# Optimization experiments

Hardware: AMD Instinct MI355X
Metric: run time of the kernel (lower is better)

## Reference

```python
import jax, jax.numpy as jnp
import numpy as np

B, S, D, H, DFF = 4, 1024, 1024, 16, 4096
MAX_LEN = 1024
DK = D // H
EPS = 1e-5


def _ln(x, g, b):
    m = jnp.mean(x, axis=-1, keepdims=True)
    v = jnp.mean(jnp.square(x - m), axis=-1, keepdims=True)
    return (x - m) / jnp.sqrt(v + EPS) * g + b


def setup_inputs() -> dict:
    key = jax.random.key(0)
    ks = jax.random.split(key, 16)
    s = 0.02
    inp = {
        "x": jax.random.normal(ks[0], (B, S, D), jnp.float32),
        "wq": jax.random.normal(ks[1], (D, D), jnp.float32) * s,
        "bq": jnp.zeros((D,), jnp.float32),
        "wk": jax.random.normal(ks[2], (D, D), jnp.float32) * s,
        "bk": jnp.zeros((D,), jnp.float32),
        "wv": jax.random.normal(ks[3], (D, D), jnp.float32) * s,
        "bv": jnp.zeros((D,), jnp.float32),
        "wo": jax.random.normal(ks[4], (D, D), jnp.float32) * s,
        "bo": jnp.zeros((D,), jnp.float32),
        "rel_table": jax.random.normal(ks[5], (2 * MAX_LEN - 1, H), jnp.float32) * s,
        "ln1_g": jnp.ones((D,), jnp.float32),
        "ln1_b": jnp.zeros((D,), jnp.float32),
        "w1": jax.random.normal(ks[6], (D, DFF), jnp.float32) * s,
        "b1": jnp.zeros((DFF,), jnp.float32),
        "w2": jax.random.normal(ks[7], (DFF, D), jnp.float32) * s,
        "b2": jnp.zeros((D,), jnp.float32),
        "ln2_g": jnp.ones((D,), jnp.float32),
        "ln2_b": jnp.zeros((D,), jnp.float32),
        "mask": jnp.ones((B, 1, 1, S), jnp.int32),
    }
    return inp


def reference(x, wq, bq, wk, bk, wv, bv, wo, bo, rel_table,
              ln1_g, ln1_b, w1, b1, w2, b2, ln2_g, ln2_b, mask):
    # --- multi-head attention with relative position bias (post-LN encoder layer, eval mode) ---
    q = (x @ wq + bq).reshape(B, S, H, DK).transpose(0, 2, 1, 3)  # [B,H,S,dk]
    k = (x @ wk + bk).reshape(B, S, H, DK).transpose(0, 2, 1, 3)
    v = (x @ wv + bv).reshape(B, S, H, DK).transpose(0, 2, 1, 3)

    scores = jnp.einsum('bhqd,bhkd->bhqk', q, k) / jnp.sqrt(jnp.float32(DK))

    # relative position bias: table[(q - k + max_len - 1).clip] -> [1,H,S,S]
    coords = jnp.arange(S)[:, None] - jnp.arange(S)[None, :] + (MAX_LEN - 1)
    coords = jnp.clip(coords, 0, 2 * MAX_LEN - 2)
    bias = rel_table[coords]              # [S,S,H]
    scores = scores + bias.transpose(2, 0, 1)[None]

    scores = jnp.where(mask == 0, jnp.float32(-1e9), scores)
    attn = jax.nn.softmax(scores, axis=-1)
    ctx = jnp.einsum('bhqk,bhkd->bhqd', attn, v)
    ctx = ctx.transpose(0, 2, 1, 3).reshape(B, S, D)
    attn_out = ctx @ wo + bo

    x1 = _ln(x + attn_out, ln1_g, ln1_b)

    ff = jax.nn.relu(x1 @ w1 + b1) @ w2 + b2
    return _ln(x1 + ff, ln2_g, ln2_b)
```

## Files before the change

kernel.cpp:

```cpp
#include <hip/hip_runtime.h>
#include <hip/hip_bf16.h>

typedef __hip_bfloat16 bf16;
typedef __attribute__((ext_vector_type(8))) short short8;
typedef __attribute__((ext_vector_type(4))) float f32x4;

#define LOG2E 1.4426950408889634f

typedef const __attribute__((address_space(1))) void* gptr_t;
typedef __attribute__((address_space(3))) void* sptr_t;

__device__ __forceinline__ void async16(void* lds, const void* g) {
  __builtin_amdgcn_global_load_lds((gptr_t)g, (sptr_t)lds, 16, 0, 0);
}

__device__ __forceinline__ float bf2f(unsigned short u) {
  union { unsigned int i; float f; } c; c.i = ((unsigned int)u) << 16; return c.f;
}


__global__ __launch_bounds__(256) void cast_f2b_kernel(
    const float* __restrict__ src, bf16* __restrict__ dst, int n) {
  int i = (blockIdx.x * 256 + threadIdx.x) * 4;
  if (i >= n) return;
  float4 v = *(const float4*)(src + i);
  bf16 h4[4] = {__float2bfloat16(v.x), __float2bfloat16(v.y),
                __float2bfloat16(v.z), __float2bfloat16(v.w)};
  *(uint2*)((unsigned short*)dst + i) = *(uint2*)h4;
}

__global__ __launch_bounds__(256) void concat_bias(
    const float* __restrict__ bq, const float* __restrict__ bk,
    const float* __restrict__ bv, float* __restrict__ o) {
  int i = blockIdx.x * 256 + threadIdx.x;
  if (i >= 3072) return;
  o[i] = (i < 1024) ? bq[i] : (i < 2048 ? bk[i - 1024] : bv[i - 2048]);
}

__global__ __launch_bounds__(256) void transpose_f2b(
    const float* __restrict__ src, bf16* __restrict__ dst, int K, int N) {
  __shared__ float tl[32][33];
  int n0 = blockIdx.x * 32, k0 = blockIdx.y * 32;
  int tx = threadIdx.x, ty = threadIdx.y;
#pragma unroll
  for (int j = 0; j < 4; ++j)
    tl[ty + j * 8][tx] = src[(size_t)(k0 + ty + j * 8) * N + n0 + tx];
  __syncthreads();
#pragma unroll
  for (int j = 0; j < 4; ++j)
    dst[(size_t)(n0 + ty + j * 8) * K + k0 + tx] =
        __float2bfloat16(tl[tx][ty + j * 8]);
}

__global__ __launch_bounds__(256) void transpose4_f2b(
    const float* __restrict__ s0, const float* __restrict__ s1,
    const float* __restrict__ s2, const float* __restrict__ s3,
    bf16* __restrict__ d0, bf16* __restrict__ d1,
    bf16* __restrict__ d2, bf16* __restrict__ d3) {
  __shared__ float tl[32][33];
  const int z = blockIdx.z;
  const float* src = z == 0 ? s0 : z == 1 ? s1 : z == 2 ? s2 : s3;
  bf16* dst = z == 0 ? d0 : z == 1 ? d1 : z == 2 ? d2 : d3;
  int n0 = blockIdx.x * 32, k0 = blockIdx.y * 32;
  int tx = threadIdx.x, ty = threadIdx.y;
#pragma unroll
  for (int j = 0; j < 4; ++j)
    tl[ty + j * 8][tx] = src[(size_t)(k0 + ty + j * 8) * 1024 + n0 + tx];
  __syncthreads();
#pragma unroll
  for (int j = 0; j < 4; ++j)
    dst[(size_t)(n0 + ty + j * 8) * 1024 + k0 + tx] =
        __float2bfloat16(tl[tx][ty + j * 8]);
}

__global__ __launch_bounds__(256) void build_vt(
    const bf16* __restrict__ qkv, bf16* __restrict__ vt) {
  __shared__ bf16 tl[32][33];
  const int bhz = blockIdx.z, s0 = blockIdx.x * 32, dk0 = blockIdx.y * 32;
  const int b = bhz >> 4, h = bhz & 15;
  const int tx = threadIdx.x, ty = threadIdx.y;
#pragma unroll
  for (int j = 0; j < 4; ++j) {
    int s = s0 + ty + j * 8;
    tl[ty + j * 8][tx] =
        qkv[(size_t)(b * 1024 + s) * 3072 + 2048 + h * 64 + dk0 + tx];
  }
  __syncthreads();
#pragma unroll
  for (int j = 0; j < 4; ++j) {
    int dk = dk0 + ty + j * 8;
    vt[(size_t)(bhz * 64 + dk) * 1024 + s0 + tx] = tl[tx][ty + j * 8];
  }
}


template <int RELU>
__global__ __launch_bounds__(256) void gemm_bt(
    const bf16* __restrict__ A, const bf16* __restrict__ Bt,
    const float* __restrict__ bias, bf16* __restrict__ C, int M, int N, int K) {
  __shared__ bf16 As[128 * 64];
  __shared__ bf16 Bs[128 * 64];
  const int t = threadIdx.x;
  const int w = t >> 6, l = t & 63;
  const int m0 = blockIdx.y * 128, n0 = blockIdx.x * 128;
  const int wr = (w >> 1) * 64, wc = (w & 1) * 64;
  const int srow = l >> 3, scol = l & 7;
  const int lm = l & 15, lq = l >> 4;

  f32x4 acc[4][4];
#pragma unroll
  for (int i = 0; i < 4; ++i)
#pragma unroll
    for (int j = 0; j < 4; ++j) acc[i][j] = (f32x4){0.f, 0.f, 0.f, 0.f};

  for (int k0 = 0; k0 < K; k0 += 64) {
#pragma unroll
    for (int p = 0; p < 4; ++p) {
      int row = p * 32 + w * 8 + srow;
      int gc = scol ^ (row & 7);
      async16(&As[(p * 32 + w * 8) * 64], A + (size_t)(m0 + row) * K + k0 + gc * 8);
      async16(&Bs[(p * 32 + w * 8) * 64], Bt + (size_t)(n0 + row) * K + k0 + gc * 8);
    }
    __syncthreads();
#pragma unroll
    for (int kk = 0; kk < 2; ++kk) {
      short8 af[4], bfr[4];
#pragma unroll
      for (int mi = 0; mi < 4; ++mi) {
        int row = wr + mi * 16 + lm;
        int c = kk * 4 + lq;
        af[mi] = *(const short8*)&As[row * 64 + ((c ^ (row & 7)) << 3)];
      }
#pragma unroll
      for (int ni = 0; ni < 4; ++ni) {
        int row = wc + ni * 16 + lm;
        int c = kk * 4 + lq;
        bfr[ni] = *(const short8*)&Bs[row * 64 + ((c ^ (row & 7)) << 3)];
      }
#pragma unroll
      for (int mi = 0; mi < 4; ++mi)
#pragma unroll
        for (int ni = 0; ni < 4; ++ni)
          acc[mi][ni] = __builtin_amdgcn_mfma_f32_16x16x32_bf16(
              af[mi], bfr[ni], acc[mi][ni], 0, 0, 0);
    }
    __syncthreads();
  }
#pragma unroll
  for (int mi = 0; mi < 4; ++mi)
#pragma unroll
    for (int r = 0; r < 4; ++r) {
      int row = m0 + wr + mi * 16 + lq * 4 + r;
#pragma unroll
      for (int ni = 0; ni < 4; ++ni) {
        int col = n0 + wc + ni * 16 + lm;
        float v = acc[mi][ni][r] + bias[col];
        if (RELU) v = fmaxf(v, 0.f);
        C[(size_t)row * N + col] = __float2bfloat16(v);
      }
    }
}

template <typename OT>
__global__ __launch_bounds__(256) void gemm_bt_splitk(
    const bf16* __restrict__ A, const bf16* __restrict__ Bt,
    OT* __restrict__ P, int M, int N, int lda, int KS) {
  __shared__ bf16 As[128 * 64];
  __shared__ bf16 Bs[128 * 64];
  const int t = threadIdx.x;
  const int w = t >> 6, l = t & 63;
  const int m0 = blockIdx.y * 128, n0 = blockIdx.x * 128;
  const int kstart = blockIdx.z * KS;
  const int wr = (w >> 1) * 64, wc = (w & 1) * 64;
  const int srow = l >> 3, scol = l & 7;
  const int lm = l & 15, lq = l >> 4;

  f32x4 acc[4][4];
#pragma unroll
  for (int i = 0; i < 4; ++i)
#pragma unroll
    for (int j = 0; j < 4; ++j) acc[i][j] = (f32x4){0.f, 0.f, 0.f, 0.f};

  for (int k0 = kstart; k0 < kstart + KS; k0 += 64) {
#pragma unroll
    for (int p = 0; p < 4; ++p) {
      int row = p * 32 + w * 8 + srow;
      int gc = scol ^ (row & 7);
      async16(&As[(p * 32 + w * 8) * 64], A + (size_t)(m0 + row) * lda + k0 + gc * 8);
      async16(&Bs[(p * 32 + w * 8) * 64], Bt + (size_t)(n0 + row) * lda + k0 + gc * 8);
    }
    __syncthreads();
#pragma unroll
    for (int kk = 0; kk < 2; ++kk) {
      short8 af[4], bfr[4];
#pragma unroll
      for (int mi = 0; mi < 4; ++mi) {
        int row = wr + mi * 16 + lm;
        int c = kk * 4 + lq;
        af[mi] = *(const short8*)&As[row * 64 + ((c ^ (row & 7)) << 3)];
      }
#pragma unroll
      for (int ni = 0; ni < 4; ++ni) {
        int row = wc + ni * 16 + lm;
        int c = kk * 4 + lq;
        bfr[ni] = *(const short8*)&Bs[row * 64 + ((c ^ (row & 7)) << 3)];
      }
#pragma unroll
      for (int mi = 0; mi < 4; ++mi)
#pragma unroll
        for (int ni = 0; ni < 4; ++ni)
          acc[mi][ni] = __builtin_amdgcn_mfma_f32_16x16x32_bf16(
              af[mi], bfr[ni], acc[mi][ni], 0, 0, 0);
    }
    __syncthreads();
  }
  OT* Pz = P + (size_t)blockIdx.z * M * N;
#pragma unroll
  for (int mi = 0; mi < 4; ++mi)
#pragma unroll
    for (int r = 0; r < 4; ++r) {
      int row = m0 + wr + mi * 16 + lq * 4 + r;
#pragma unroll
      for (int ni = 0; ni < 4; ++ni) {
        int col = n0 + wc + ni * 16 + lm;
        float v = acc[mi][ni][r];
        if constexpr (sizeof(OT) == 4)
          Pz[(size_t)row * N + col] = v;
        else
          Pz[(size_t)row * N + col] = __float2bfloat16(v);
      }
    }
}


__global__ __launch_bounds__(256) void flash_attn(
    const bf16* __restrict__ qkv, const bf16* __restrict__ vt,
    const float* __restrict__ rel, const int* __restrict__ mask,
    bf16* __restrict__ ctx) {
  __shared__ bf16 Kl[64 * 64];
  __shared__ bf16 Vl[64 * 64];
  __shared__ bf16 Pl[128 * 72];
  __shared__ float bias_s[192];
  __shared__ float mask_s[64];
  __shared__ float alpha_s[128];
  __shared__ float linv_s[128];

  const int t = threadIdx.x;
  const int w = t >> 6, l = t & 63;
  const int lm = l & 15, lq = l >> 4;
  const int qt = blockIdx.x, bh = blockIdx.y;
  const int b = bh >> 4, h = bh & 15;
  const int q0 = qt * 128;

  {
    int srow = l >> 3, scol = l & 7;
#pragma unroll
    for (int p = 0; p < 4; ++p) {
      int row = p * 32 + w * 8 + srow;
      int gc = scol ^ (row & 7);
      async16(&Pl[(p * 32 + w * 8) * 64],
              qkv + (size_t)(b * 1024 + q0 + row) * 3072 + h * 64 + gc * 8);
    }
  }
  __syncthreads();
  short8 qf[2][2];
#pragma unroll
  for (int ni = 0; ni < 2; ++ni)
#pragma unroll
    for (int kk = 0; kk < 2; ++kk) {
      int row = w * 32 + ni * 16 + lm;
      int c = kk * 4 + lq;
      qf[ni][kk] = *(const short8*)&Pl[row * 64 + ((c ^ (row & 7)) << 3)];
    }
  __syncthreads();

  float m_st[2] = {-1e30f, -1e30f};
  float l_st[2] = {0.f, 0.f};
  f32x4 acc_o[2][4];
#pragma unroll
  for (int i = 0; i < 2; ++i)
#pragma unroll
    for (int j = 0; j < 4; ++j) acc_o[i][j] = (f32x4){0.f, 0.f, 0.f, 0.f};

  for (int kt = 0; kt < 16; ++kt) {
    const int k0 = kt * 64;
    {
      int srow = l >> 3, scol = l & 7;
#pragma unroll
      for (int p = 0; p < 2; ++p) {
        int row = p * 32 + w * 8 + srow;
        int gc = scol ^ (row & 7);
        async16(&Kl[(p * 32 + w * 8) * 64],
                qkv + (size_t)(b * 1024 + k0 + row) * 3072 + 1024 + h * 64 + gc * 8);
        async16(&Vl[(p * 32 + w * 8) * 64],
                vt + (size_t)(bh * 64 + row) * 1024 + k0 + gc * 8);
      }
    }
    if (t < 191) bias_s[t] = rel[(q0 - k0 + 960 + t) * 16 + h];
    if (t < 64) mask_s[t] = (mask[b * 1024 + k0 + t] == 0) ? -1e9f : 0.f;
    __syncthreads();

    f32x4 sa[4][2];
#pragma unroll
    for (int i = 0; i < 4; ++i)
#pragma unroll
      for (int j = 0; j < 2; ++j) sa[i][j] = (f32x4){0.f, 0.f, 0.f, 0.f};
#pragma unroll
    for (int kk = 0; kk < 2; ++kk) {
      short8 ak[4];
#pragma unroll
      for (int mi = 0; mi < 4; ++mi) {
        int row = mi * 16 + lm;
        int c = kk * 4 + lq;
        ak[mi] = *(const short8*)&Kl[row * 64 + ((c ^ (row & 7)) << 3)];
      }
#pragma unroll
      for (int mi = 0; mi < 4; ++mi)
#pragma unroll
        for (int ni = 0; ni < 2; ++ni)
          sa[mi][ni] = __builtin_amdgcn_mfma_f32_16x16x32_bf16(
              ak[mi], qf[ni][kk], sa[mi][ni], 0, 0, 0);
    }

    float mloc[2] = {-1e30f, -1e30f};
#pragma unroll
    for (int mi = 0; mi < 4; ++mi)
#pragma unroll
      for (int r = 0; r < 4; ++r) {
        int kl = mi * 16 + lq * 4 + r;
        float mk = mask_s[kl];
        int bi = w * 32 + lm - kl + 63;
#pragma unroll
        for (int ni = 0; ni < 2; ++ni) {
          float v = sa[mi][ni][r] * 0.125f + bias_s[bi + ni * 16] + mk;
          sa[mi][ni][r] = v;
          mloc[ni] = fmaxf(mloc[ni], v);
        }
      }
    float alpha[2];
#pragma unroll
    for (int ni = 0; ni < 2; ++ni) {
      mloc[ni] = fmaxf(mloc[ni], __shfl_xor(mloc[ni], 16));
      mloc[ni] = fmaxf(mloc[ni], __shfl_xor(mloc[ni], 32));
      float mn = fmaxf(m_st[ni], mloc[ni]);
      alpha[ni] = exp2f((m_st[ni] - mn) * LOG2E);
      m_st[ni] = mn;
    }
    float ls[2] = {0.f, 0.f};
#pragma unroll
    for (int mi = 0; mi < 4; ++mi)
#pragma unroll
      for (int ni = 0; ni < 2; ++ni)
#pragma unroll
        for (int r = 0; r < 4; ++r) {
          float p = exp2f((sa[mi][ni][r] - m_st[ni]) * LOG2E);
          sa[mi][ni][r] = p;
          ls[ni] += p;
        }
#pragma unroll
    for (int ni = 0; ni < 2; ++ni) {
      ls[ni] += __shfl_xor(ls[ni], 16);
      ls[ni] += __shfl_xor(ls[ni], 32);
      l_st[ni] = l_st[ni] * alpha[ni] + ls[ni];
    }
    if (lq == 0) {
      alpha_s[w * 32 + lm] = alpha[0];
      alpha_s[w * 32 + 16 + lm] = alpha[1];
    }
#pragma unroll
    for (int mi = 0; mi < 4; ++mi)
#pragma unroll
      for (int ni = 0; ni < 2; ++ni) {
        bf16 h4[4];
#pragma unroll
        for (int r = 0; r < 4; ++r) h4[r] = __float2bfloat16(sa[mi][ni][r]);
        int q = w * 32 + ni * 16 + lm;
        int sk = mi * 16 + lq * 4;
        *(uint2*)&Pl[q * 72 + sk] = *(uint2*)h4;
      }
    __syncthreads();

#pragma unroll
    for (int mi2 = 0; mi2 < 2; ++mi2)
#pragma unroll
      for (int r = 0; r < 4; ++r) {
        float a = alpha_s[w * 32 + mi2 * 16 + lq * 4 + r];
#pragma unroll
        for (int ni = 0; ni < 4; ++ni) acc_o[mi2][ni][r] *= a;
      }
#pragma unroll
    for (int kk2 = 0; kk2 < 2; ++kk2) {
      short8 pf[2];
#pragma unroll
      for (int mi2 = 0; mi2 < 2; ++mi2) {
        int q = w * 32 + mi2 * 16 + lm;
        pf[mi2] = *(const short8*)&Pl[q * 72 + kk2 * 32 + lq * 8];
      }
      short8 vf[4];
#pragma unroll
      for (int ni = 0; ni < 4; ++ni) {
        int dk = ni * 16 + lm;
        int c = kk2 * 4 + lq;
        vf[ni] = *(const short8*)&Vl[dk * 64 + ((c ^ (dk & 7)) << 3)];
      }
#pragma unroll
      for (int mi2 = 0; mi2 < 2; ++mi2)
#pragma unroll
        for (int ni = 0; ni < 4; ++ni)
          acc_o[mi2][ni] = __builtin_amdgcn_mfma_f32_16x16x32_bf16(
              pf[mi2], vf[ni], acc_o[mi2][ni], 0, 0, 0);
    }
    __syncthreads();
  }

  if (lq == 0) {
    linv_s[w * 32 + lm] = 1.f / l_st[0];
    linv_s[w * 32 + 16 + lm] = 1.f / l_st[1];
  }
  __syncthreads();
#pragma unroll
  for (int mi2 = 0; mi2 < 2; ++mi2)
#pragma unroll
    for (int r = 0; r < 4; ++r) {
      int qx = w * 32 + mi2 * 16 + lq * 4 + r;
      float inv = linv_s[qx];
      size_t rowbase = (size_t)(b * 1024 + q0 + qx) * 1024 + h * 64;
#pragma unroll
      for (int ni = 0; ni < 4; ++ni)
        ctx[rowbase + ni * 16 + lm] = __float2bfloat16(acc_o[mi2][ni][r] * inv);
    }
}


template <typename PT, int NS>
__global__ __launch_bounds__(256) void ln_resid(
    const float* __restrict__ xin, const PT* __restrict__ part,
    const float* __restrict__ bias,
    const float* __restrict__ gw, const float* __restrict__ bw,
    float* __restrict__ outf, bf16* __restrict__ outb) {
  const int row = blockIdx.x, t = threadIdx.x;
  const size_t base = (size_t)row * 1024 + t * 4;
  float4 xv = *(const float4*)(xin + base);
  float4 bi = *(const float4*)(bias + t * 4);
  float v0 = xv.x + bi.x, v1 = xv.y + bi.y, v2 = xv.z + bi.z, v3 = xv.w + bi.w;
#pragma unroll
  for (int s = 0; s < NS; ++s) {
    const PT* p = part + (size_t)s * 4194304 + base;
    if constexpr (sizeof(PT) == 4) {
      float4 pv = *(const float4*)p;
      v0 += pv.x; v1 += pv.y; v2 += pv.z; v3 += pv.w;
    } else {
      ushort4 pv = *(const ushort4*)p;
      v0 += bf2f(pv.x); v1 += bf2f(pv.y); v2 += bf2f(pv.z); v3 += bf2f(pv.w);
    }
  }
  float s1 = v0 + v1 + v2 + v3;
  float s2 = v0 * v0 + v1 * v1 + v2 * v2 + v3 * v3;
#pragma unroll
  for (int o = 1; o < 64; o <<= 1) {
    s1 += __shfl_xor(s1, o);
    s2 += __shfl_xor(s2, o);
  }
  __shared__ float red[8];
  const int w = t >> 6, l = t & 63;
  if (l == 0) { red[w] = s1; red[4 + w] = s2; }
  __syncthreads();
  float S1 = red[0] + red[1] + red[2] + red[3];
  float S2 = red[4] + red[5] + red[6] + red[7];
  float mean = S1 * (1.f / 1024.f);
  float var = S2 * (1.f / 1024.f) - mean * mean;
  float rstd = rsqrtf(var + 1e-5f);
  float4 gv = *(const float4*)(gw + t * 4);
  float4 bv = *(const float4*)(bw + t * 4);
  float o0 = (v0 - mean) * rstd * gv.x + bv.x;
  float o1 = (v1 - mean) * rstd * gv.y + bv.y;
  float o2 = (v2 - mean) * rstd * gv.z + bv.z;
  float o3 = (v3 - mean) * rstd * gv.w + bv.w;
  if (outf) {
    float4 ov = {o0, o1, o2, o3};
    *(float4*)(outf + base) = ov;
  }
  if (outb) {
    bf16 h4[4] = {__float2bfloat16(o0), __float2bfloat16(o1),
                  __float2bfloat16(o2), __float2bfloat16(o3)};
    *(uint2*)((unsigned short*)outb + base) = *(uint2*)h4;
  }
}


extern "C" void kernel_launch(void* const* d_in, const int* in_sizes, int n_in,
                              void* d_out, int out_size, void* d_ws, size_t ws_size,
                              hipStream_t stream) {
  (void)in_sizes; (void)n_in; (void)out_size; (void)ws_size;
  const float* x   = (const float*)d_in[0];
  const float* wq  = (const float*)d_in[1];
  const float* bq  = (const float*)d_in[2];
  const float* wk  = (const float*)d_in[3];
  const float* bk  = (const float*)d_in[4];
  const float* wv  = (const float*)d_in[5];
  const float* bv  = (const float*)d_in[6];
  const float* wo  = (const float*)d_in[7];
  const float* bo  = (const float*)d_in[8];
  const float* rel = (const float*)d_in[9];
  const float* g1  = (const float*)d_in[10];
  const float* be1 = (const float*)d_in[11];
  const float* w1  = (const float*)d_in[12];
  const float* b1  = (const float*)d_in[13];
  const float* w2  = (const float*)d_in[14];
  const float* b2  = (const float*)d_in[15];
  const float* g2  = (const float*)d_in[16];
  const float* be2 = (const float*)d_in[17];
  const int* mask  = (const int*)d_in[18];
  float* out = (float*)d_out;

  char* ws = (char*)d_ws;
  bf16*  xb      = (bf16*)(ws + 0);
  bf16*  wqkv_t  = (bf16*)(ws + 8388608);
  bf16*  wo_t    = (bf16*)(ws + 14680064);
  bf16*  w1_t    = (bf16*)(ws + 16777216);
  bf16*  ctx_b   = (bf16*)(ws + 25165824);
  bf16*  x1b     = (bf16*)(ws + 33554432);
  bf16*  qkv_b   = (bf16*)(ws + 41943040);
  bf16*  vtb     = (bf16*)(ws + 67108864);
  float* part_wo = (float*)(ws + 41943040);
  bf16*  h1      = (bf16*)(ws + 41943040);
  bf16*  part_ff = (bf16*)(ws + 0);
  bf16*  w2_t    = (bf16*)(ws + 75497472);
  float* x1f     = (float*)(ws + 83886080);
  float* bqkv    = (float*)(ws + 100663296);

  dim3 tb(32, 8);
  cast_f2b_kernel<<<4096, 256, 0, stream>>>(x, xb, 4096 * 1024);
  concat_bias<<<12, 256, 0, stream>>>(bq, bk, bv, bqkv);
  transpose4_f2b<<<dim3(32, 32, 4), tb, 0, stream>>>(
      wq, wk, wv, wo, wqkv_t, wqkv_t + 1024 * 1024, wqkv_t + 2048 * 1024, wo_t);
  transpose_f2b<<<dim3(128, 32), tb, 0, stream>>>(w1, w1_t, 1024, 4096);
  transpose_f2b<<<dim3(32, 128), tb, 0, stream>>>(w2, w2_t, 4096, 1024);

  gemm_bt<0><<<dim3(24, 32), 256, 0, stream>>>(xb, wqkv_t, bqkv, qkv_b, 4096, 3072, 1024);
  build_vt<<<dim3(32, 2, 64), tb, 0, stream>>>(qkv_b, vtb);
  flash_attn<<<dim3(8, 64), 256, 0, stream>>>(qkv_b, vtb, rel, mask, ctx_b);
  gemm_bt_splitk<float><<<dim3(8, 32, 2), 256, 0, stream>>>(
      ctx_b, wo_t, part_wo, 4096, 1024, 1024, 512);
  ln_resid<float, 2><<<4096, 256, 0, stream>>>(x, part_wo, bo, g1, be1, x1f, x1b);
  gemm_bt<1><<<dim3(32, 32), 256, 0, stream>>>(x1b, w1_t, b1, h1, 4096, 4096, 1024);
  gemm_bt_splitk<bf16><<<dim3(8, 32, 4), 256, 0, stream>>>(
      h1, w2_t, part_ff, 4096, 1024, 4096, 1024);
  ln_resid<bf16, 4><<<4096, 256, 0, stream>>>(x1f, part_ff, b2, g2, be2, out, nullptr);
}
```

Measured before the change: 379.0 us.

## Double-buffer K/V tiles in flash attention and use 8 waves of 16 queries

The flash attention kernel now runs 512 threads: each of 8 waves owns 16 query rows instead of 32. K, V, bias and mask tiles are double-buffered so the next tile's async loads are issued before the current tile is computed, leaving one barrier per iteration. The LOG2E factor is folded into the score scale, bias and mask so the raw hardware exp2 can be used. Per-row alpha and 1/l are passed by shuffles instead of shared memory, and the P tile uses an XOR swizzle instead of padding. This aims to hide load latency and cut barriers and LDS traffic, at the cost of more LDS per block and higher register pressure from the launch bound.

Result: faster. 360.3 us (-4.9%).

```diff
diff --git a/kernel.cpp b/kernel.cpp
--- a/kernel.cpp
+++ b/kernel.cpp
@@ -233,17 +233,15 @@
 }
 
 
-__global__ __launch_bounds__(256) void flash_attn(
+__global__ __launch_bounds__(512, 4) void flash_attn(
     const bf16* __restrict__ qkv, const bf16* __restrict__ vt,
     const float* __restrict__ rel, const int* __restrict__ mask,
     bf16* __restrict__ ctx) {
-  __shared__ bf16 Kl[64 * 64];
-  __shared__ bf16 Vl[64 * 64];
-  __shared__ bf16 Pl[128 * 72];
-  __shared__ float bias_s[192];
-  __shared__ float mask_s[64];
-  __shared__ float alpha_s[128];
-  __shared__ float linv_s[128];
+  __shared__ bf16 Kl[2][64 * 64];
+  __shared__ bf16 Vl[2][64 * 64];
+  __shared__ bf16 Pl[128 * 64];
+  __shared__ float bias_s[2][192];
+  __shared__ float mask_s[2][64];
 
   const int t = threadIdx.x;
   const int w = t >> 6, l = t & 63;
@@ -251,184 +249,134 @@
   const int qt = blockIdx.x, bh = blockIdx.y;
   const int b = bh >> 4, h = bh & 15;
   const int q0 = qt * 128;
-
-  {
-    int srow = l >> 3, scol = l & 7;
-#pragma unroll
-    for (int p = 0; p < 4; ++p) {
-      int row = p * 32 + w * 8 + srow;
-      int gc = scol ^ (row & 7);
-      async16(&Pl[(p * 32 + w * 8) * 64],
-              qkv + (size_t)(b * 1024 + q0 + row) * 3072 + h * 64 + gc * 8);
-    }
-  }
-  __syncthreads();
-  short8 qf[2][2];
-#pragma unroll
-  for (int ni = 0; ni < 2; ++ni)
-#pragma unroll
-    for (int kk = 0; kk < 2; ++kk) {
-      int row = w * 32 + ni * 16 + lm;
-      int c = kk * 4 + lq;
-      qf[ni][kk] = *(const short8*)&Pl[row * 64 + ((c ^ (row & 7)) << 3)];
-    }
-  __syncthreads();
-
-  float m_st[2] = {-1e30f, -1e30f};
-  float l_st[2] = {0.f, 0.f};
-  f32x4 acc_o[2][4];
-#pragma unroll
-  for (int i = 0; i < 2; ++i)
-#pragma unroll
-    for (int j = 0; j < 4; ++j) acc_o[i][j] = (f32x4){0.f, 0.f, 0.f, 0.f};
+  const int srow = l >> 3;
+  const int gc = (l & 7) ^ srow;
+  const int qq = w * 16 + lm;
+
+  auto stage = [&](int d, int k0n) {
+    async16(&Kl[d][w * 8 * 64],
+            qkv + (size_t)(b * 1024 + k0n + w * 8 + srow) * 3072 + 1024 + h * 64 + gc * 8);
+    async16(&Vl[d][w * 8 * 64],
+            vt + ((size_t)bh * 64 + w * 8 + srow) * 1024 + k0n + gc * 8);
+    if (t < 191) bias_s[d][t] = rel[(q0 - k0n + 960 + t) * 16 + h] * LOG2E;
+    if (t < 64) mask_s[d][t] = (mask[b * 1024 + k0n + t] == 0) ? -1.44e9f : 0.f;
+  };
+
+#pragma unroll
+  for (int p = 0; p < 2; ++p)
+    async16(&Pl[(p * 64 + w * 8) * 64],
+            qkv + (size_t)(b * 1024 + q0 + p * 64 + w * 8 + srow) * 3072 + h * 64 + gc * 8);
+  stage(0, 0);
+  __syncthreads();
+
+  short8 qf[2];
+#pragma unroll
+  for (int kk = 0; kk < 2; ++kk)
+    qf[kk] = *(const short8*)&Pl[qq * 64 + (((kk * 4 + lq) ^ (lm & 7)) << 3)];
+  __syncthreads();
+
+  float m_st = -1e30f, l_st = 0.f;
+  f32x4 acc_o[4];
+#pragma unroll
+  for (int j = 0; j < 4; ++j) acc_o[j] = (f32x4){0.f, 0.f, 0.f, 0.f};
+
+  const float C0 = 0.125f * LOG2E;
 
   for (int kt = 0; kt < 16; ++kt) {
-    const int k0 = kt * 64;
-    {
-      int srow = l >> 3, scol = l & 7;
-#pragma unroll
-      for (int p = 0; p < 2; ++p) {
-        int row = p * 32 + w * 8 + srow;
-        int gc = scol ^ (row & 7);
-        async16(&Kl[(p * 32 + w * 8) * 64],
-                qkv + (size_t)(b * 1024 + k0 + row) * 3072 + 1024 + h * 64 + gc * 8);
-        async16(&Vl[(p * 32 + w * 8) * 64],
-                vt + (size_t)(bh * 64 + row) * 1024 + k0 + gc * 8);
-      }
-    }
-    if (t < 191) bias_s[t] = rel[(q0 - k0 + 960 + t) * 16 + h];
-    if (t < 64) mask_s[t] = (mask[b * 1024 + k0 + t] == 0) ? -1e9f : 0.f;
-    __syncthreads();
-
-    f32x4 sa[4][2];
-#pragma unroll
-    for (int i = 0; i < 4; ++i)
-#pragma unroll
-      for (int j = 0; j < 2; ++j) sa[i][j] = (f32x4){0.f, 0.f, 0.f, 0.f};
+    const int d = kt & 1;
+    if (kt < 15) stage(d ^ 1, (kt + 1) * 64);
+
+    f32x4 sa[4];
+#pragma unroll
+    for (int i = 0; i < 4; ++i) sa[i] = (f32x4){0.f, 0.f, 0.f, 0.f};
 #pragma unroll
     for (int kk = 0; kk < 2; ++kk) {
       short8 ak[4];
 #pragma unroll
       for (int mi = 0; mi < 4; ++mi) {
         int row = mi * 16 + lm;
-        int c = kk * 4 + lq;
-        ak[mi] = *(const short8*)&Kl[row * 64 + ((c ^ (row & 7)) << 3)];
+        ak[mi] = *(const short8*)&Kl[d][row * 64 + (((kk * 4 + lq) ^ (lm & 7)) << 3)];
       }
 #pragma unroll
       for (int mi = 0; mi < 4; ++mi)
-#pragma unroll
-        for (int ni = 0; ni < 2; ++ni)
-          sa[mi][ni] = __builtin_amdgcn_mfma_f32_16x16x32_bf16(
-              ak[mi], qf[ni][kk], sa[mi][ni], 0, 0, 0);
-    }
-
-    float mloc[2] = {-1e30f, -1e30f};
+        sa[mi] = __builtin_amdgcn_mfma_f32_16x16x32_bf16(ak[mi], qf[kk], sa[mi], 0, 0, 0);
+    }
+
+    float m4[4][4];
+#pragma unroll
+    for (int mi = 0; mi < 4; ++mi)
+      *(float4*)m4[mi] = *(const float4*)&mask_s[d][mi * 16 + lq * 4];
+    float mx = -1e30f;
 #pragma unroll
     for (int mi = 0; mi < 4; ++mi)
 #pragma unroll
       for (int r = 0; r < 4; ++r) {
         int kl = mi * 16 + lq * 4 + r;
-        float mk = mask_s[kl];
-        int bi = w * 32 + lm - kl + 63;
-#pragma unroll
-        for (int ni = 0; ni < 2; ++ni) {
-          float v = sa[mi][ni][r] * 0.125f + bias_s[bi + ni * 16] + mk;
-          sa[mi][ni][r] = v;
-          mloc[ni] = fmaxf(mloc[ni], v);
-        }
-      }
-    float alpha[2];
-#pragma unroll
-    for (int ni = 0; ni < 2; ++ni) {
-      mloc[ni] = fmaxf(mloc[ni], __shfl_xor(mloc[ni], 16));
-      mloc[ni] = fmaxf(mloc[ni], __shfl_xor(mloc[ni], 32));
-      float mn = fmaxf(m_st[ni], mloc[ni]);
-      alpha[ni] = exp2f((m_st[ni] - mn) * LOG2E);
-      m_st[ni] = mn;
-    }
-    float ls[2] = {0.f, 0.f};
+        float v = sa[mi][r] * C0 + (bias_s[d][qq - kl + 63] + m4[mi][r]);
+        sa[mi][r] = v;
+        mx = fmaxf(mx, v);
+      }
+    mx = fmaxf(mx, __shfl_xor(mx, 16));
+    mx = fmaxf(mx, __shfl_xor(mx, 32));
+    float mn = fmaxf(m_st, mx);
+    float alpha = __builtin_amdgcn_exp2f(m_st - mn);
+    m_st = mn;
+    float ls = 0.f;
 #pragma unroll
     for (int mi = 0; mi < 4; ++mi)
 #pragma unroll
-      for (int ni = 0; ni < 2; ++ni)
-#pragma unroll
-        for (int r = 0; r < 4; ++r) {
-          float p = exp2f((sa[mi][ni][r] - m_st[ni]) * LOG2E);
-          sa[mi][ni][r] = p;
-          ls[ni] += p;
-        }
-#pragma unroll
-    for (int ni = 0; ni < 2; ++ni) {
-      ls[ni] += __shfl_xor(ls[ni], 16);
-      ls[ni] += __shfl_xor(ls[ni], 32);
-      l_st[ni] = l_st[ni] * alpha[ni] + ls[ni];
-    }
-    if (lq == 0) {
-      alpha_s[w * 32 + lm] = alpha[0];
-      alpha_s[w * 32 + 16 + lm] = alpha[1];
-    }
-#pragma unroll
-    for (int mi = 0; mi < 4; ++mi)
-#pragma unroll
-      for (int ni = 0; ni < 2; ++ni) {
-        bf16 h4[4];
-#pragma unroll
-        for (int r = 0; r < 4; ++r) h4[r] = __float2bfloat16(sa[mi][ni][r]);
-        int q = w * 32 + ni * 16 + lm;
-        int sk = mi * 16 + lq * 4;
-        *(uint2*)&Pl[q * 72 + sk] = *(uint2*)h4;
-      }
+      for (int r = 0; r < 4; ++r) {
+        float p = __builtin_amdgcn_exp2f(sa[mi][r] - mn);
+        sa[mi][r] = p;
+        ls += p;
+      }
+    ls += __shfl_xor(ls, 16);
+    ls += __shfl_xor(ls, 32);
+    l_st = l_st * alpha + ls;
+
+#pragma unroll
+    for (int mi = 0; mi < 4; ++mi) {
+      bf16 h4[4];
+#pragma unroll
+      for (int r = 0; r < 4; ++r) h4[r] = __float2bfloat16(sa[mi][r]);
+      int chunk = mi * 2 + (lq >> 1);
+      *(uint2*)&Pl[qq * 64 + ((chunk ^ (lm & 7)) << 3) + ((lq & 1) << 2)] =
+          *(uint2*)h4;
+    }
+
+#pragma unroll
+    for (int r = 0; r < 4; ++r) {
+      float a = __shfl(alpha, lq * 4 + r);
+#pragma unroll
+      for (int ni = 0; ni < 4; ++ni) acc_o[ni][r] *= a;
+    }
+
+#pragma unroll
+    for (int kk2 = 0; kk2 < 2; ++kk2) {
+      short8 pf = *(const short8*)&Pl[qq * 64 + (((kk2 * 4 + lq) ^ (lm & 7)) << 3)];
+      short8 vf[4];
+#pragma unroll
+      for (int ni = 0; ni < 4; ++ni) {
+        int rowv = ni * 16 + lm;
+        vf[ni] = *(const short8*)&Vl[d][rowv * 64 + (((kk2 * 4 + lq) ^ (lm & 7)) << 3)];
+      }
+#pragma unroll
+      for (int ni = 0; ni < 4; ++ni)
+        acc_o[ni] = __builtin_amdgcn_mfma_f32_16x16x32_bf16(pf, vf[ni], acc_o[ni], 0, 0, 0);
+    }
     __syncthreads();
-
-#pragma unroll
-    for (int mi2 = 0; mi2 < 2; ++mi2)
-#pragma unroll
-      for (int r = 0; r < 4; ++r) {
-        float a = alpha_s[w * 32 + mi2 * 16 + lq * 4 + r];
-#pragma unroll
-        for (int ni = 0; ni < 4; ++ni) acc_o[mi2][ni][r] *= a;
-      }
-#pragma unroll
-    for (int kk2 = 0; kk2 < 2; ++kk2) {
-      short8 pf[2];
-#pragma unroll
-      for (int mi2 = 0; mi2 < 2; ++mi2) {
-        int q = w * 32 + mi2 * 16 + lm;
-        pf[mi2] = *(const short8*)&Pl[q * 72 + kk2 * 32 + lq * 8];
-      }
-      short8 vf[4];
-#pragma unroll
-      for (int ni = 0; ni < 4; ++ni) {
-        int dk = ni * 16 + lm;
-        int c = kk2 * 4 + lq;
-        vf[ni] = *(const short8*)&Vl[dk * 64 + ((c ^ (dk & 7)) << 3)];
-      }
-#pragma unroll
-      for (int mi2 = 0; mi2 < 2; ++mi2)
-#pragma unroll
-        for (int ni = 0; ni < 4; ++ni)
-          acc_o[mi2][ni] = __builtin_amdgcn_mfma_f32_16x16x32_bf16(
-              pf[mi2], vf[ni], acc_o[mi2][ni], 0, 0, 0);
-    }
-    __syncthreads();
-  }
-
-  if (lq == 0) {
-    linv_s[w * 32 + lm] = 1.f / l_st[0];
-    linv_s[w * 32 + 16 + lm] = 1.f / l_st[1];
-  }
-  __syncthreads();
-#pragma unroll
-  for (int mi2 = 0; mi2 < 2; ++mi2)
-#pragma unroll
-    for (int r = 0; r < 4; ++r) {
-      int qx = w * 32 + mi2 * 16 + lq * 4 + r;
-      float inv = linv_s[qx];
-      size_t rowbase = (size_t)(b * 1024 + q0 + qx) * 1024 + h * 64;
-#pragma unroll
-      for (int ni = 0; ni < 4; ++ni)
-        ctx[rowbase + ni * 16 + lm] = __float2bfloat16(acc_o[mi2][ni][r] * inv);
-    }
+  }
+
+  float linv = 1.f / l_st;
+#pragma unroll
+  for (int r = 0; r < 4; ++r) {
+    float il = __shfl(linv, lq * 4 + r);
+    int qx = w * 16 + lq * 4 + r;
+    size_t rowbase = (size_t)(b * 1024 + q0 + qx) * 1024 + h * 64;
+#pragma unroll
+    for (int ni = 0; ni < 4; ++ni)
+      ctx[rowbase + ni * 16 + lm] = __float2bfloat16(acc_o[ni][r] * il);
+  }
 }
 
 
@@ -539,7 +487,7 @@
 
   gemm_bt<0><<<dim3(24, 32), 256, 0, stream>>>(xb, wqkv_t, bqkv, qkv_b, 4096, 3072, 1024);
   build_vt<<<dim3(32, 2, 64), tb, 0, stream>>>(qkv_b, vtb);
-  flash_attn<<<dim3(8, 64), 256, 0, stream>>>(qkv_b, vtb, rel, mask, ctx_b);
+  flash_attn<<<dim3(8, 64), 512, 0, stream>>>(qkv_b, vtb, rel, mask, ctx_b);
   gemm_bt_splitk<float><<<dim3(8, 32, 2), 256, 0, stream>>>(
       ctx_b, wo_t, part_wo, 4096, 1024, 1024, 512);
   ln_resid<float, 2><<<4096, 256, 0, stream>>>(x, part_wo, bo, g1, be1, x1f, x1b);
```
